# Performance work log

Hardware: AMD Instinct MI355X
Metric: run time of the kernel (lower is better)

## Reference

```python
import jax, jax.numpy as jnp
import numpy as np

# Keras ConvLSTM2D defaults: activation=tanh, recurrent_activation=hard_sigmoid,
# gate order i, f, c, o; padding='same'; BatchNormalization: axis=-1, eps=1e-3.

def hard_sigmoid(x):
    return jnp.clip(0.2 * x + 0.5, 0.0, 1.0)

def conv2d(x, w):
    # x: (N, H, W, Cin), w: (kh, kw, Cin, Cout), stride 1, SAME padding
    return jax.lax.conv_general_dilated(
        x, w, window_strides=(1, 1), padding='SAME',
        dimension_numbers=('NHWC', 'HWIO', 'NHWC'))

def conv_lstm(x_seq, Wx, Wh, b):
    # x_seq: (B, T, H, W, Cin); Wx: (k,k,Cin,4F); Wh: (k,k,F,4F); b: (4F,)
    B, T, H, W, Cin = x_seq.shape
    F = Wh.shape[2]
    # Input-to-gate convs are time-independent: do all T steps as one batched conv.
    xg = conv2d(x_seq.reshape(B * T, H, W, Cin), Wx).reshape(B, T, H, W, 4 * F) + b
    xg = jnp.moveaxis(xg, 1, 0)  # (T, B, H, W, 4F)
    h0 = jnp.zeros((B, H, W, F), x_seq.dtype)

    def step(carry, g_in):
        h, c = carry
        g = g_in + conv2d(h, Wh)  # (B, H, W, 4F)
        i, f, cc, o = jnp.split(g, 4, axis=-1)
        i = hard_sigmoid(i)
        f = hard_sigmoid(f)
        o = hard_sigmoid(o)
        c = f * c + i * jnp.tanh(cc)
        h = o * jnp.tanh(c)
        return (h, c), h

    (h, c), ys = jax.lax.scan(step, (h0, h0), xg)
    return jnp.moveaxis(ys, 0, 1), h, c  # (B,T,H,W,F), (B,H,W,F), (B,H,W,F)

def batchnorm_train(x, gamma, beta, eps=1e-3):
    # training=True: batch statistics over all axes but channels (biased var)
    mean = jnp.mean(x, axis=(0, 1, 2, 3), keepdims=True)
    var = jnp.var(x, axis=(0, 1, 2, 3), keepdims=True)
    return gamma * (x - mean) * jax.lax.rsqrt(var + eps) + beta

def setup_inputs() -> dict:
    key = jax.random.key(0)
    ks = jax.random.split(key, 9)
    B, T, H, W, Cin, F, k = 8, 10, 48, 48, 16, 64, 3
    s = 0.05
    return {
        'x':      jax.random.normal(ks[0], (B, T, H, W, Cin), jnp.float32),
        'Wx1':    jax.random.normal(ks[1], (k, k, Cin, 4 * F), jnp.float32) * s,
        'Wh1':    jax.random.normal(ks[2], (k, k, F, 4 * F), jnp.float32) * s,
        'b1':     jnp.zeros((4 * F,), jnp.float32),
        'gamma1': jnp.ones((F,), jnp.float32),
        'beta1':  jnp.zeros((F,), jnp.float32),
        'Wx2':    jax.random.normal(ks[3], (k, k, F, 4 * F), jnp.float32) * s,
        'Wh2':    jax.random.normal(ks[4], (k, k, F, 4 * F), jnp.float32) * s,
        'b2':     jnp.zeros((4 * F,), jnp.float32),
    }

def reference(x, Wx1, Wh1, b1, gamma1, beta1, Wx2, Wh2, b2):
    seq1, h1, c1 = conv_lstm(x, Wx1, Wh1, b1)
    seq1 = batchnorm_train(seq1, gamma1, beta1)
    _, h2, c2 = conv_lstm(seq1, Wx2, Wh2, b2)
    # states = [[h1, c1], [h2, c2]] flattened
    return (h1, c1, h2, c2)
```

## Files before the change

### kernel.cpp

```cpp
#include <hip/hip_runtime.h>
#include <hip/hip_bf16.h>

typedef short bf16x8 __attribute__((ext_vector_type(8)));
typedef float f32x4  __attribute__((ext_vector_type(4)));

constexpr int B = 8, T = 10, F = 64, CO = 256;
constexpr long IMGPIX      = 48 * 48;
constexpr long STATE_ELEMS = (long)B * IMGPIX * F;
constexpr float BN_INVN    = 1.0f / (float)(B * T * IMGPIX);

__device__ __forceinline__ float  b2f(ushort u) { return __uint_as_float(((unsigned)u) << 16); }
__device__ __forceinline__ ushort f2b(float f) {
    unsigned x = __float_as_uint(f);
    return (ushort)((x + 0x7fffu + ((x >> 16) & 1u)) >> 16);
}
__device__ __forceinline__ float hsig(float x) { return fminf(fmaxf(0.2f * x + 0.5f, 0.f), 1.f); }
__device__ __forceinline__ float tanh_f(float v) {
    return 1.f - 2.f / (__expf(2.f * v) + 1.f);
}

union V16 { uint4 u; bf16x8 b; };

template<int CIN_A, int CPAD, int KSHARD>
__device__ __forceinline__ void mfma_loop(
    const unsigned char* __restrict__ smem,
    const unsigned char* __restrict__ pA,
    const ushort* __restrict__ Wsw,
    int q, int l, f32x4 (&acc)[3][4])
{
    constexpr int KX  = 9 * CIN_A;
    constexpr int KSX = (KX + 31) / 32;
    constexpr int KS  = KSX + 18;
    constexpr int ITERS = (KS - KSHARD + 1) / 2;
    const int lm  = l & 15;
    const int lk8 = (l >> 4) * 8;

#pragma unroll
    for (int ksl = 0; ksl < ITERS; ++ksl) {
        const int ks = 2 * ksl + KSHARD;
        V16 bf[4];
#pragma unroll
        for (int nr = 0; nr < 4; ++nr) {
            const int ntile = nr * 4 + q;
            bf[nr].u = *(const uint4*)(Wsw + ((size_t)((ntile * KS + ks) * 64) + l) * 8);
        }
        V16 af[3];
        if (CIN_A == 64 || ks >= KSX) {
            const int base_ch = (CIN_A == 64 && ks < KSX) ? 0 : CIN_A;
            const int khs     = (CIN_A == 64 && ks < KSX) ? ks : ks - KSX;
            const int tap = khs >> 1;
            const int ky = tap / 3, kx = tap - 3 * (tap / 3);
            const int ch = base_ch + (khs & 1) * 32;
#pragma unroll
            for (int m = 0; m < 3; ++m) {
                const int IMM = ((ky * 50 + kx + m * 16) * CPAD + ch) * 2;
                af[m].u = *(const uint4*)(pA + IMM);
            }
        } else {
            const int k = ks * 32 + lk8;
            const bool valid = (k < KX);
            const int tap = valid ? (2 * ks + (lk8 >> 4)) : 0;
            const int ky = tap / 3, kx = tap - 3 * (tap / 3);
            const int dci = (lk8 & 16) * 2;
#pragma unroll
            for (int m = 0; m < 3; ++m) {
                const int base = ((ky * 50 + kx + m * 16) * CPAD) * 2;
                uint4 v = *(const uint4*)(pA + (valid ? base - dci : 0));
                if (!valid) v = make_uint4(0, 0, 0, 0);
                af[m].u = v;
            }
        }
#pragma unroll
        for (int m = 0; m < 3; ++m)
#pragma unroll
            for (int nr = 0; nr < 4; ++nr)
                acc[m][nr] = __builtin_amdgcn_mfma_f32_16x16x32_bf16(
                    af[m].b, bf[nr].b, acc[m][nr], 0, 0, 0);
    }
}

template<int CIN_A, int CPAD, bool FIRST, bool STATS, bool BNIN, bool OUT>
__global__ __launch_bounds__(256, 3) void convlstm_step(
    const ushort* __restrict__ inA, long strideA,
    const ushort* __restrict__ inB,
    const ushort* __restrict__ Wsw,
    const float*  __restrict__ bias,
    float*  __restrict__ cState,
    ushort* __restrict__ hOut,
    ushort* __restrict__ seqOut,
    float*  __restrict__ stats,
    const float* __restrict__ gamma,
    const float* __restrict__ beta,
    float*  __restrict__ outF)
{
    constexpr int CIN_TOT = CIN_A + 64;
    constexpr int PATCHB = 3 * 50 * CPAD * 2;
    constexpr int SMEMB  = PATCHB > 26368 ? PATCHB : 26368;
    __shared__ __align__(16) unsigned char smem[SMEMB];
    __shared__ float bnsc[64], bnsh[64];

    const int bid  = blockIdx.x;
    const int img  = bid / 96;
    const int rem  = bid % 96;
    const int y    = rem >> 1;
    const int half = rem & 1;
    const int tid = threadIdx.x, wid = tid >> 6, l = tid & 63;
    const int lm = l & 15, lk8 = (l >> 4) * 8;

    if constexpr (BNIN) {
        if (tid < 64) {
            const float mean = stats[tid] * BN_INVN;
            const float var  = stats[64 + tid] * BN_INVN - mean * mean;
            const float sc   = gamma[tid] * rsqrtf(var + 1e-3f);
            bnsc[tid] = sc;
            bnsh[tid] = beta[tid] - mean * sc;
        }
        __syncthreads();
    }

    const ushort* aBase = inA + (size_t)img * strideA;
    const ushort* bBase = inB + (size_t)img * IMGPIX * 64;
    constexpr int CA8 = CIN_A / 8;
    for (int e = tid; e < 3 * 48 * CA8; e += 256) {
        const int r = e / (48 * CA8), qq = e % (48 * CA8);
        const int col = qq / CA8, ci0 = (qq % CA8) * 8;
        const int gy = y + r - 1;
        uint4 v = make_uint4(0, 0, 0, 0);
        if (gy >= 0 && gy < 48) {
            v = *(const uint4*)(aBase + ((size_t)gy * 48 + col) * CIN_A + ci0);
            if constexpr (BNIN) {
                ushort* u = (ushort*)&v;
#pragma unroll
                for (int j = 0; j < 8; ++j)
                    u[j] = f2b(b2f(u[j]) * bnsc[ci0 + j] + bnsh[ci0 + j]);
            }
        }
        *(uint4*)(smem + ((r * 50 + col + 1) * CPAD + ci0) * 2) = v;
    }
    for (int e = tid; e < 3 * 48 * 8; e += 256) {
        const int r = e / (48 * 8), qq = e % (48 * 8);
        const int col = qq / 8, ci0 = (qq % 8) * 8;
        uint4 v = make_uint4(0, 0, 0, 0);
        if constexpr (!FIRST) {
            const int gy = y + r - 1;
            if (gy >= 0 && gy < 48)
                v = *(const uint4*)(bBase + ((size_t)gy * 48 + col) * 64 + ci0);
        }
        *(uint4*)(smem + ((r * 50 + col + 1) * CPAD + CIN_A + ci0) * 2) = v;
    }
    constexpr int CT8 = CIN_TOT / 8;
    for (int e = tid; e < 3 * 2 * CT8; e += 256) {
        const int r = e / (2 * CT8), qq = e % (2 * CT8);
        const int dc = (qq / CT8) ? 49 : 0, ci0 = (qq % CT8) * 8;
        *(uint4*)(smem + ((r * 50 + dc) * CPAD + ci0) * 2) = make_uint4(0, 0, 0, 0);
    }
    __syncthreads();

    const int q      = 2 * half + (wid & 1);
    const int kshard = wid >> 1;
    const unsigned char* pA = smem + (lm * CPAD + lk8) * 2;

    f32x4 acc[3][4] = {};
    if (kshard == 0) mfma_loop<CIN_A, CPAD, 0>(smem, pA, Wsw, q, l, acc);
    else             mfma_loop<CIN_A, CPAD, 1>(smem, pA, Wsw, q, l, acc);

    __syncthreads();
    float* gbuf = (float*)smem;
    float* sred = (float*)(smem + 25344);
    const int fl = (q & 1) * 16 + lm;

    if (kshard == 0) {
#pragma unroll
        for (int nr = 0; nr < 4; ++nr) {
            const float bv = bias[nr * 64 + q * 16 + lm];
#pragma unroll
            for (int m = 0; m < 3; ++m)
#pragma unroll
                for (int r = 0; r < 4; ++r) {
                    const int pixel = m * 16 + (l >> 4) * 4 + r;
                    gbuf[pixel * 132 + nr * 32 + fl] = acc[m][nr][r] + bv;
                }
        }
    }
    __syncthreads();
    if (kshard == 1) {
#pragma unroll
        for (int nr = 0; nr < 4; ++nr)
#pragma unroll
            for (int m = 0; m < 3; ++m)
#pragma unroll
                for (int r = 0; r < 4; ++r) {
                    const int pixel = m * 16 + (l >> 4) * 4 + r;
                    gbuf[pixel * 132 + nr * 32 + fl] += acc[m][nr][r];
                }
    }
    __syncthreads();

    float s1 = 0.f, s2 = 0.f;
    const size_t rowBase = (size_t)img * IMGPIX + (size_t)y * 48;
#pragma unroll
    for (int it = 0; it < 6; ++it) {
        const int idx = it * 256 + tid;
        const int p = idx >> 5, fr = idx & 31;
        const float gi = gbuf[p * 132 + fr];
        const float gf = gbuf[p * 132 + 32 + fr];
        const float gc = gbuf[p * 132 + 64 + fr];
        const float go = gbuf[p * 132 + 96 + fr];
        const size_t off = (rowBase + p) * 64 + half * 32 + fr;
        const float cold = FIRST ? 0.f : cState[off];
        const float cn = hsig(gf) * cold + hsig(gi) * tanh_f(gc);
        const float hn = hsig(go) * tanh_f(cn);
        cState[off] = cn;
        hOut[off]   = f2b(hn);
        if constexpr (STATS) { seqOut[off] = f2b(hn); s1 += hn; s2 += hn * hn; }
        if constexpr (OUT)   { outF[off] = hn; outF[STATE_ELEMS + off] = cn; }
    }

    if constexpr (STATS) {
        s1 += __shfl_xor(s1, 32);
        s2 += __shfl_xor(s2, 32);
        if (l < 32) { sred[wid * 64 + l] = s1; sred[wid * 64 + 32 + l] = s2; }
        __syncthreads();
        if (tid < 64) {
            const int kind = tid >> 5, fr = tid & 31;
            const float v = sred[kind * 32 + fr] + sred[64 + kind * 32 + fr]
                          + sred[128 + kind * 32 + fr] + sred[192 + kind * 32 + fr];
            atomicAdd(&stats[kind * 64 + half * 32 + fr], v);
        }
    }
}

__device__ __forceinline__ ushort swz_elem_seg(
    const float* __restrict__ Wx, const float* __restrict__ Wh,
    int CIN_A, int idx)
{
    const int KX = 9 * CIN_A, KSX = (KX + 31) / 32, KS = KSX + 18;
    const int j = idx & 7, lw = (idx >> 3) & 63, rest = idx >> 9;
    const int ks = rest % KS, ntile = rest / KS;
    const int n = ntile * 16 + (lw & 15);
    const int k = ks * 32 + ((lw >> 4) & 3) * 8 + j;
    float v = 0.f;
    if (ks < KSX) {
        if (k < KX) {
            const int tap = k / CIN_A, ci = k % CIN_A;
            v = Wx[((size_t)tap * CIN_A + ci) * CO + n];
        }
    } else {
        const int kh = k - KSX * 32;
        const int tap = kh >> 6, ci = kh & 63;
        v = Wh[((size_t)tap * 64 + ci) * CO + n];
    }
    return f2b(v);
}

__global__ __launch_bounds__(256) void prep_kernel(
    const float* __restrict__ x,
    const float* __restrict__ Wx1, const float* __restrict__ Wh1,
    const float* __restrict__ Wx2, const float* __restrict__ Wh2,
    ushort* __restrict__ xb, ushort* __restrict__ wc1, ushort* __restrict__ wc2,
    float* __restrict__ stats)
{
    constexpr int N0 = 368640;
    constexpr int N1 = 16 * 23 * 512;
    constexpr int N2 = 16 * 36 * 512;
    const int gid = blockIdx.x * 256 + threadIdx.x;
    if (gid < N0) {
        const float4 a = ((const float4*)x)[(size_t)gid * 2];
        const float4 b = ((const float4*)x)[(size_t)gid * 2 + 1];
        ushort o[8] = { f2b(a.x), f2b(a.y), f2b(a.z), f2b(a.w),
                        f2b(b.x), f2b(b.y), f2b(b.z), f2b(b.w) };
        *(uint4*)(xb + (size_t)gid * 8) = *(const uint4*)o;
    } else if (gid < N0 + N1) {
        wc1[gid - N0] = swz_elem_seg(Wx1, Wh1, 16, gid - N0);
    } else if (gid < N0 + N1 + N2) {
        wc2[gid - N0 - N1] = swz_elem_seg(Wx2, Wh2, 64, gid - N0 - N1);
    } else if (gid < N0 + N1 + N2 + 128) {
        stats[gid - N0 - N1 - N2] = 0.f;
    }
}

extern "C" void kernel_launch(void* const* d_in, const int* in_sizes, int n_in,
                              void* d_out, int out_size, void* d_ws, size_t ws_size,
                              hipStream_t stream)
{
    const float* x      = (const float*)d_in[0];
    const float* Wx1    = (const float*)d_in[1];
    const float* Wh1    = (const float*)d_in[2];
    const float* b1     = (const float*)d_in[3];
    const float* gamma1 = (const float*)d_in[4];
    const float* beta1  = (const float*)d_in[5];
    const float* Wx2    = (const float*)d_in[6];
    const float* Wh2    = (const float*)d_in[7];
    const float* b2     = (const float*)d_in[8];

    unsigned char* w = (unsigned char*)d_ws;
    ushort* seq1 = (ushort*)w;  w += 23592960;
    ushort* xb   = (ushort*)w;  w += 5898240;
    ushort* wc1  = (ushort*)w;  w += 376832;
    ushort* wc2  = (ushort*)w;  w += 589824;
    ushort* hb1a = (ushort*)w;  w += 2359296;
    ushort* hb1b = (ushort*)w;  w += 2359296;
    ushort* hb2a = (ushort*)w;  w += 2359296;
    ushort* hb2b = (ushort*)w;  w += 2359296;
    float*  c1   = (float*)w;   w += 4718592;
    float*  c2   = (float*)w;   w += 4718592;
    float*  stats = (float*)w;  w += 512;

    prep_kernel<<<3329, 256, 0, stream>>>(x, Wx1, Wh1, Wx2, Wh2, xb, wc1, wc2, stats);

    const long xStride = (long)T * IMGPIX * 16;
    ushort* hp1[2] = { hb1a, hb1b };

    convlstm_step<16, 88, true, true, false, false><<<768, 256, 0, stream>>>(
        xb, xStride, hp1[0], wc1, b1, c1, hp1[1],
        seq1, stats, nullptr, nullptr, nullptr);
    for (int t = 1; t < 9; ++t)
        convlstm_step<16, 88, false, true, false, false><<<768, 256, 0, stream>>>(
            xb + (size_t)t * IMGPIX * 16, xStride, hp1[t & 1], wc1, b1, c1, hp1[(t + 1) & 1],
            seq1 + (size_t)t * STATE_ELEMS, stats, nullptr, nullptr, nullptr);
    convlstm_step<16, 88, false, true, false, true><<<768, 256, 0, stream>>>(
        xb + (size_t)9 * IMGPIX * 16, xStride, hp1[1], wc1, b1, c1, hp1[0],
        seq1 + (size_t)9 * STATE_ELEMS, stats, nullptr, nullptr, (float*)d_out);

    ushort* hp2[2] = { hb2a, hb2b };
    convlstm_step<64, 136, true, false, true, false><<<768, 256, 0, stream>>>(
        seq1, IMGPIX * 64, hp2[0], wc2, b2, c2, hp2[1],
        nullptr, stats, gamma1, beta1, nullptr);
    for (int t = 1; t < 9; ++t)
        convlstm_step<64, 136, false, false, true, false><<<768, 256, 0, stream>>>(
            seq1 + (size_t)t * STATE_ELEMS, IMGPIX * 64, hp2[t & 1], wc2, b2, c2, hp2[(t + 1) & 1],
            nullptr, stats, gamma1, beta1, nullptr);
    convlstm_step<64, 136, false, false, true, true><<<768, 256, 0, stream>>>(
        seq1 + (size_t)9 * STATE_ELEMS, IMGPIX * 64, hp2[1], wc2, b2, c2, hp2[0],
        nullptr, stats, gamma1, beta1, (float*)d_out + 2 * STATE_ELEMS);
}
```

Baseline: 413.1 us.

## Drop K-split across waves and apply LSTM gates directly from MFMA registers

Blocks shrink from four waves to two, and each wave now runs the full K reduction for its column tile instead of splitting K into two shards. Since all four gates for a given feature sit in one wave's accumulators, the LSTM update is computed straight from registers. This removes the shared-memory gate buffer, the cross-shard reduction and several barriers. The cost is half as many waves per block, so less latency hiding inside a block, and a longer serial MFMA chain per wave. The stats reduction now uses shuffles and more atomics.

```diff
diff --git a/kernel.cpp b/kernel.cpp
--- a/kernel.cpp
+++ b/kernel.cpp
@@ -21,9 +21,8 @@
 
 union V16 { uint4 u; bf16x8 b; };
 
-template<int CIN_A, int CPAD, int KSHARD>
+template<int CIN_A, int CPAD>
 __device__ __forceinline__ void mfma_loop(
-    const unsigned char* __restrict__ smem,
     const unsigned char* __restrict__ pA,
     const ushort* __restrict__ Wsw,
     int q, int l, f32x4 (&acc)[3][4])
@@ -31,13 +30,10 @@
     constexpr int KX  = 9 * CIN_A;
     constexpr int KSX = (KX + 31) / 32;
     constexpr int KS  = KSX + 18;
-    constexpr int ITERS = (KS - KSHARD + 1) / 2;
-    const int lm  = l & 15;
     const int lk8 = (l >> 4) * 8;
 
 #pragma unroll
-    for (int ksl = 0; ksl < ITERS; ++ksl) {
-        const int ks = 2 * ksl + KSHARD;
+    for (int ks = 0; ks < KS; ++ks) {
         V16 bf[4];
 #pragma unroll
         for (int nr = 0; nr < 4; ++nr) {
@@ -80,7 +76,7 @@
 }
 
 template<int CIN_A, int CPAD, bool FIRST, bool STATS, bool BNIN, bool OUT>
-__global__ __launch_bounds__(256, 3) void convlstm_step(
+__global__ __launch_bounds__(128) void convlstm_step(
     const ushort* __restrict__ inA, long strideA,
     const ushort* __restrict__ inB,
     const ushort* __restrict__ Wsw,
@@ -95,8 +91,7 @@
 {
     constexpr int CIN_TOT = CIN_A + 64;
     constexpr int PATCHB = 3 * 50 * CPAD * 2;
-    constexpr int SMEMB  = PATCHB > 26368 ? PATCHB : 26368;
-    __shared__ __align__(16) unsigned char smem[SMEMB];
+    __shared__ __align__(16) unsigned char smem[PATCHB];
     __shared__ float bnsc[64], bnsh[64];
 
     const int bid  = blockIdx.x;
@@ -121,7 +116,7 @@
     const ushort* aBase = inA + (size_t)img * strideA;
     const ushort* bBase = inB + (size_t)img * IMGPIX * 64;
     constexpr int CA8 = CIN_A / 8;
-    for (int e = tid; e < 3 * 48 * CA8; e += 256) {
+    for (int e = tid; e < 3 * 48 * CA8; e += 128) {
         const int r = e / (48 * CA8), qq = e % (48 * CA8);
         const int col = qq / CA8, ci0 = (qq % CA8) * 8;
         const int gy = y + r - 1;
@@ -137,7 +132,7 @@
         }
         *(uint4*)(smem + ((r * 50 + col + 1) * CPAD + ci0) * 2) = v;
     }
-    for (int e = tid; e < 3 * 48 * 8; e += 256) {
+    for (int e = tid; e < 3 * 48 * 8; e += 128) {
         const int r = e / (48 * 8), qq = e % (48 * 8);
         const int col = qq / 8, ci0 = (qq % 8) * 8;
         uint4 v = make_uint4(0, 0, 0, 0);
@@ -149,83 +144,51 @@
         *(uint4*)(smem + ((r * 50 + col + 1) * CPAD + CIN_A + ci0) * 2) = v;
     }
     constexpr int CT8 = CIN_TOT / 8;
-    for (int e = tid; e < 3 * 2 * CT8; e += 256) {
+    for (int e = tid; e < 3 * 2 * CT8; e += 128) {
         const int r = e / (2 * CT8), qq = e % (2 * CT8);
         const int dc = (qq / CT8) ? 49 : 0, ci0 = (qq % CT8) * 8;
         *(uint4*)(smem + ((r * 50 + dc) * CPAD + ci0) * 2) = make_uint4(0, 0, 0, 0);
     }
     __syncthreads();
 
-    const int q      = 2 * half + (wid & 1);
-    const int kshard = wid >> 1;
+    const int q = 2 * half + wid;
     const unsigned char* pA = smem + (lm * CPAD + lk8) * 2;
 
     f32x4 acc[3][4] = {};
-    if (kshard == 0) mfma_loop<CIN_A, CPAD, 0>(smem, pA, Wsw, q, l, acc);
-    else             mfma_loop<CIN_A, CPAD, 1>(smem, pA, Wsw, q, l, acc);
-
-    __syncthreads();
-    float* gbuf = (float*)smem;
-    float* sred = (float*)(smem + 25344);
-    const int fl = (q & 1) * 16 + lm;
-
-    if (kshard == 0) {
-#pragma unroll
-        for (int nr = 0; nr < 4; ++nr) {
-            const float bv = bias[nr * 64 + q * 16 + lm];
-#pragma unroll
-            for (int m = 0; m < 3; ++m)
-#pragma unroll
-                for (int r = 0; r < 4; ++r) {
-                    const int pixel = m * 16 + (l >> 4) * 4 + r;
-                    gbuf[pixel * 132 + nr * 32 + fl] = acc[m][nr][r] + bv;
-                }
-        }
-    }
-    __syncthreads();
-    if (kshard == 1) {
-#pragma unroll
-        for (int nr = 0; nr < 4; ++nr)
-#pragma unroll
-            for (int m = 0; m < 3; ++m)
-#pragma unroll
-                for (int r = 0; r < 4; ++r) {
-                    const int pixel = m * 16 + (l >> 4) * 4 + r;
-                    gbuf[pixel * 132 + nr * 32 + fl] += acc[m][nr][r];
-                }
-    }
-    __syncthreads();
+    mfma_loop<CIN_A, CPAD>(pA, Wsw, q, l, acc);
+
+    const float bv_i = bias[      q * 16 + lm];
+    const float bv_f = bias[ 64 + q * 16 + lm];
+    const float bv_c = bias[128 + q * 16 + lm];
+    const float bv_o = bias[192 + q * 16 + lm];
 
     float s1 = 0.f, s2 = 0.f;
     const size_t rowBase = (size_t)img * IMGPIX + (size_t)y * 48;
 #pragma unroll
-    for (int it = 0; it < 6; ++it) {
-        const int idx = it * 256 + tid;
-        const int p = idx >> 5, fr = idx & 31;
-        const float gi = gbuf[p * 132 + fr];
-        const float gf = gbuf[p * 132 + 32 + fr];
-        const float gc = gbuf[p * 132 + 64 + fr];
-        const float go = gbuf[p * 132 + 96 + fr];
-        const size_t off = (rowBase + p) * 64 + half * 32 + fr;
-        const float cold = FIRST ? 0.f : cState[off];
-        const float cn = hsig(gf) * cold + hsig(gi) * tanh_f(gc);
-        const float hn = hsig(go) * tanh_f(cn);
-        cState[off] = cn;
-        hOut[off]   = f2b(hn);
-        if constexpr (STATS) { seqOut[off] = f2b(hn); s1 += hn; s2 += hn * hn; }
-        if constexpr (OUT)   { outF[off] = hn; outF[STATE_ELEMS + off] = cn; }
-    }
+    for (int m = 0; m < 3; ++m)
+#pragma unroll
+        for (int r = 0; r < 4; ++r) {
+            const int p = m * 16 + (l >> 4) * 4 + r;
+            const float gi = acc[m][0][r] + bv_i;
+            const float gf = acc[m][1][r] + bv_f;
+            const float gc = acc[m][2][r] + bv_c;
+            const float go = acc[m][3][r] + bv_o;
+            const size_t off = (rowBase + p) * 64 + q * 16 + lm;
+            const float cold = FIRST ? 0.f : cState[off];
+            const float cn = hsig(gf) * cold + hsig(gi) * tanh_f(gc);
+            const float hn = hsig(go) * tanh_f(cn);
+            cState[off] = cn;
+            hOut[off]   = f2b(hn);
+            if constexpr (STATS) { seqOut[off] = f2b(hn); s1 += hn; s2 += hn * hn; }
+            if constexpr (OUT)   { outF[off] = hn; outF[STATE_ELEMS + off] = cn; }
+        }
 
     if constexpr (STATS) {
-        s1 += __shfl_xor(s1, 32);
-        s2 += __shfl_xor(s2, 32);
-        if (l < 32) { sred[wid * 64 + l] = s1; sred[wid * 64 + 32 + l] = s2; }
-        __syncthreads();
-        if (tid < 64) {
-            const int kind = tid >> 5, fr = tid & 31;
-            const float v = sred[kind * 32 + fr] + sred[64 + kind * 32 + fr]
-                          + sred[128 + kind * 32 + fr] + sred[192 + kind * 32 + fr];
-            atomicAdd(&stats[kind * 64 + half * 32 + fr], v);
+        s1 += __shfl_xor(s1, 16);  s2 += __shfl_xor(s2, 16);
+        s1 += __shfl_xor(s1, 32);  s2 += __shfl_xor(s2, 32);
+        if (l < 16) {
+            atomicAdd(&stats[     q * 16 + lm], s1);
+            atomicAdd(&stats[64 + q * 16 + lm], s2);
         }
     }
 }
@@ -311,26 +274,26 @@
     const long xStride = (long)T * IMGPIX * 16;
     ushort* hp1[2] = { hb1a, hb1b };
 
-    convlstm_step<16, 88, true, true, false, false><<<768, 256, 0, stream>>>(
+    convlstm_step<16, 88, true, true, false, false><<<768, 128, 0, stream>>>(
         xb, xStride, hp1[0], wc1, b1, c1, hp1[1],
         seq1, stats, nullptr, nullptr, nullptr);
     for (int t = 1; t < 9; ++t)
-        convlstm_step<16, 88, false, true, false, false><<<768, 256, 0, stream>>>(
+        convlstm_step<16, 88, false, true, false, false><<<768, 128, 0, stream>>>(
             xb + (size_t)t * IMGPIX * 16, xStride, hp1[t & 1], wc1, b1, c1, hp1[(t + 1) & 1],
             seq1 + (size_t)t * STATE_ELEMS, stats, nullptr, nullptr, nullptr);
-    convlstm_step<16, 88, false, true, false, true><<<768, 256, 0, stream>>>(
+    convlstm_step<16, 88, false, true, false, true><<<768, 128, 0, stream>>>(
         xb + (size_t)9 * IMGPIX * 16, xStride, hp1[1], wc1, b1, c1, hp1[0],
         seq1 + (size_t)9 * STATE_ELEMS, stats, nullptr, nullptr, (float*)d_out);
 
     ushort* hp2[2] = { hb2a, hb2b };
-    convlstm_step<64, 136, true, false, true, false><<<768, 256, 0, stream>>>(
+    convlstm_step<64, 136, true, false, true, false><<<768, 128, 0, stream>>>(
         seq1, IMGPIX * 64, hp2[0], wc2, b2, c2, hp2[1],
         nullptr, stats, gamma1, beta1, nullptr);
     for (int t = 1; t < 9; ++t)
-        convlstm_step<64, 136, false, false, true, false><<<768, 256, 0, stream>>>(
+        convlstm_step<64, 136, false, false, true, false><<<768, 128, 0, stream>>>(
             seq1 + (size_t)t * STATE_ELEMS, IMGPIX * 64, hp2[t & 1], wc2, b2, c2, hp2[(t + 1) & 1],
             nullptr, stats, gamma1, beta1, nullptr);
-    convlstm_step<64, 136, false, false, true, true><<<768, 256, 0, stream>>>(
+    convlstm_step<64, 136, false, false, true, true><<<768, 128, 0, stream>>>(
         seq1 + (size_t)9 * STATE_ELEMS, IMGPIX * 64, hp2[1], wc2, b2, c2, hp2[0],
         nullptr, stats, gamma1, beta1, (float*)d_out + 2 * STATE_ELEMS);
 }
```

New measurement: 483.9 us. +17.1%, slower.
